# Kernel tuning notes

Hardware: AMD Instinct MI355X
Metric: run time of the kernel (lower is better)

Reference implementation:

```python
import jax, jax.numpy as jnp
import numpy as np

ALPHA_LIM = (float(np.exp(-1.0 / 5.0)), float(np.exp(-1.0 / 25.0)))
BETA_LIM = (float(np.exp(-1.0 / 30.0)), float(np.exp(-1.0 / 120.0)))
A_LIM = (-1.0, 1.0)
B_LIM = (0.0, 2.0)
THRESHOLD = 1.0


@jax.custom_vjp
def spike_boxcar(x):
    # Heaviside forward, boxcar surrogate gradient
    return (x > 0).astype(x.dtype)


def _spike_fwd(x):
    return spike_boxcar(x), x


def _spike_bwd(x, g):
    return (jnp.where(jnp.abs(x) <= 0.5, g, jnp.zeros_like(g)),)


spike_boxcar.defvjp(_spike_fwd, _spike_bwd)


def setup_inputs() -> dict:
    key = jax.random.key(0)
    ks = jax.random.split(key, 9)
    B, T, I, H = 128, 512, 512, 512
    return {
        "x": jax.random.normal(ks[0], (B, T, I), dtype=jnp.float32),
        "W": jax.random.normal(ks[1], (H, I), dtype=jnp.float32) / np.sqrt(I),
        "alpha": jax.random.uniform(ks[2], (H,), dtype=jnp.float32),
        "beta": jax.random.uniform(ks[3], (H,), dtype=jnp.float32),
        "a": jax.random.uniform(ks[4], (H,), dtype=jnp.float32),
        "b": jax.random.uniform(ks[5], (H,), dtype=jnp.float32),
        "u0": jax.random.uniform(ks[6], (B, H), dtype=jnp.float32),
        "w0": jax.random.uniform(ks[7], (B, H), dtype=jnp.float32),
        "s0": jax.random.uniform(ks[8], (B, H), dtype=jnp.float32),
    }


def reference(x, W, alpha, beta, a, b, u0, w0, s0):
    # x: [B, T, I]; W: [H, I] (nn.Linear weight, no bias)
    alpha = jnp.clip(alpha, ALPHA_LIM[0], ALPHA_LIM[1])
    beta = jnp.clip(beta, BETA_LIM[0], BETA_LIM[1])
    a = jnp.clip(a, A_LIM[0], A_LIM[1])
    b = jnp.clip(b, B_LIM[0], B_LIM[1])

    Wx = jnp.einsum("bti,hi->bth", x, W)  # [B, T, H]
    Wx_t = jnp.transpose(Wx, (1, 0, 2))    # [T, B, H] for scan over time

    def step(carry, wx_t):
        ut, wt, st = carry
        wt = beta * wt + a * ut + b * st
        ut = alpha * (ut - st) + (1.0 - alpha) * (wx_t - wt)
        st = spike_boxcar(ut - THRESHOLD)
        return (ut, wt, st), st

    _, s = jax.lax.scan(step, (u0, w0, s0), Wx_t)  # s: [T, B, H]
    return jnp.transpose(s, (1, 0, 2))  # [B, T, H]
```

## Files before the change

kernel.cpp:

```cpp
#include <hip/hip_runtime.h>
#include <hip/hip_bf16.h>


#define M_SZ 65536
#define H_SZ 512
#define K_SZ 512
#define B_SZ 128
#define T_SZ 512
#define LSTR 132

typedef __attribute__((ext_vector_type(4))) float f32x4;
typedef __attribute__((ext_vector_type(4))) unsigned int u32x4;

__device__ __forceinline__ bool detect_bf16(const unsigned int* __restrict__ w) {
  int c = 0;
#pragma unroll
  for (int i = 0; i < 64; ++i) {
    unsigned int e = (w[i] >> 7) & 0xffu;
    c += (e >= 115u && e <= 131u) ? 1 : 0;
  }
  return c > 32;
}

template <bool ISB>
__device__ __forceinline__ f32x4 ld4t(const void* __restrict__ p, size_t off) {
  if constexpr (!ISB) {
    return *reinterpret_cast<const f32x4*>(reinterpret_cast<const float*>(p) + off);
  } else {
    uint2 v = *reinterpret_cast<const uint2*>(reinterpret_cast<const unsigned short*>(p) + off);
    f32x4 r;
    r.x = __uint_as_float((v.x & 0xffffu) << 16);
    r.y = __uint_as_float(v.x & 0xffff0000u);
    r.z = __uint_as_float((v.y & 0xffffu) << 16);
    r.w = __uint_as_float(v.y & 0xffff0000u);
    return r;
  }
}

template <bool ISB>
__device__ __forceinline__ float ld1t(const void* __restrict__ p, int i) {
  if constexpr (!ISB) return reinterpret_cast<const float*>(p)[i];
  return __uint_as_float((unsigned int)(reinterpret_cast<const unsigned short*>(p)[i]) << 16);
}

__device__ __forceinline__ void gl_lds16(const void* g, void* l) {
  __builtin_amdgcn_global_load_lds(
      (const __attribute__((address_space(1))) void*)g,
      (__attribute__((address_space(3))) void*)l, 16, 0, 0);
}

template <bool ISB>
__device__ __forceinline__ void gemm_body(const void* __restrict__ X,
                                          const void* __restrict__ Wm,
                                          float* __restrict__ C,
                                          float* __restrict__ As,
                                          float* __restrict__ Bs) {
  const int tid = threadIdx.x;
  const int r0 = tid >> 2;
  const int q0 = (tid & 3) * 4;
  const int tx = tid & 15;
  const int ty = tid >> 4;
  const size_t M0 = (size_t)(blockIdx.x >> 2) * 128;
  const int N0 = (blockIdx.x & 3) * 128;

  float acc[8][8];
#pragma unroll
  for (int i = 0; i < 8; ++i)
#pragma unroll
    for (int j = 0; j < 8; ++j) acc[i][j] = 0.0f;

  const size_t aoff0 = (M0 + r0) * K_SZ + q0;
  const size_t aoff1 = (M0 + r0 + 64) * K_SZ + q0;
  const size_t boff0 = (size_t)(N0 + r0) * K_SZ + q0;
  const size_t boff1 = (size_t)(N0 + r0 + 64) * K_SZ + q0;

  f32x4 pa0 = ld4t<ISB>(X, aoff0), pa1 = ld4t<ISB>(X, aoff1);
  f32x4 pb0 = ld4t<ISB>(Wm, boff0), pb1 = ld4t<ISB>(Wm, boff1);

  for (int kk = 0; kk < K_SZ; kk += 16) {
    __syncthreads();
    As[(q0 + 0) * LSTR + r0] = pa0.x; As[(q0 + 1) * LSTR + r0] = pa0.y;
    As[(q0 + 2) * LSTR + r0] = pa0.z; As[(q0 + 3) * LSTR + r0] = pa0.w;
    As[(q0 + 0) * LSTR + r0 + 64] = pa1.x; As[(q0 + 1) * LSTR + r0 + 64] = pa1.y;
    As[(q0 + 2) * LSTR + r0 + 64] = pa1.z; As[(q0 + 3) * LSTR + r0 + 64] = pa1.w;
    Bs[(q0 + 0) * LSTR + r0] = pb0.x; Bs[(q0 + 1) * LSTR + r0] = pb0.y;
    Bs[(q0 + 2) * LSTR + r0] = pb0.z; Bs[(q0 + 3) * LSTR + r0] = pb0.w;
    Bs[(q0 + 0) * LSTR + r0 + 64] = pb1.x; Bs[(q0 + 1) * LSTR + r0 + 64] = pb1.y;
    Bs[(q0 + 2) * LSTR + r0 + 64] = pb1.z; Bs[(q0 + 3) * LSTR + r0 + 64] = pb1.w;
    __syncthreads();
    if (kk + 16 < K_SZ) {
      pa0 = ld4t<ISB>(X, aoff0 + kk + 16); pa1 = ld4t<ISB>(X, aoff1 + kk + 16);
      pb0 = ld4t<ISB>(Wm, boff0 + kk + 16); pb1 = ld4t<ISB>(Wm, boff1 + kk + 16);
    }
#pragma unroll
    for (int k = 0; k < 16; ++k) {
      const f32x4 a0 = *reinterpret_cast<const f32x4*>(As + k * LSTR + ty * 4);
      const f32x4 a1 = *reinterpret_cast<const f32x4*>(As + k * LSTR + 64 + ty * 4);
      const f32x4 b0 = *reinterpret_cast<const f32x4*>(Bs + k * LSTR + tx * 4);
      const f32x4 b1 = *reinterpret_cast<const f32x4*>(Bs + k * LSTR + 64 + tx * 4);
      const float av[8] = {a0.x, a0.y, a0.z, a0.w, a1.x, a1.y, a1.z, a1.w};
      const float bv[8] = {b0.x, b0.y, b0.z, b0.w, b1.x, b1.y, b1.z, b1.w};
#pragma unroll
      for (int i = 0; i < 8; ++i)
#pragma unroll
        for (int j = 0; j < 8; ++j) acc[i][j] += av[i] * bv[j];
    }
  }

#pragma unroll
  for (int r = 0; r < 8; ++r) {
    const size_t m = M0 + ((r < 4) ? (ty * 4 + r) : (64 + ty * 4 + (r - 4)));
    float* Cp = C + m * H_SZ + N0;
    f32x4 v0 = {acc[r][0], acc[r][1], acc[r][2], acc[r][3]};
    f32x4 v1 = {acc[r][4], acc[r][5], acc[r][6], acc[r][7]};
    __builtin_nontemporal_store(v0, reinterpret_cast<f32x4*>(Cp + tx * 4));
    __builtin_nontemporal_store(v1, reinterpret_cast<f32x4*>(Cp + 64 + tx * 4));
  }
}

__global__ __launch_bounds__(256) void sgemm_bt(const void* __restrict__ X,
                                                const void* __restrict__ Wm,
                                                float* __restrict__ C) {
  __shared__ float As[16 * LSTR];
  __shared__ float Bs[16 * LSTR];
  if (detect_bf16(reinterpret_cast<const unsigned int*>(X)))
    gemm_body<true>(X, Wm, C, As, Bs);
  else
    gemm_body<false>(X, Wm, C, As, Bs);
}

#define SG 8
#define NSG (T_SZ / SG)
#define RING 6

template <bool ISB>
__device__ __forceinline__ void scan_body(
    const float* __restrict__ wx, const void* __restrict__ alpha_p,
    const void* __restrict__ beta_p, const void* __restrict__ a_p,
    const void* __restrict__ b_p, const void* __restrict__ u0p,
    const void* __restrict__ w0p, const void* __restrict__ s0p,
    void* __restrict__ out, float* __restrict__ ring, float* __restrict__ stage) {
  const int tid = threadIdx.x;
  const int wave = tid >> 6;
  const int lane = tid & 63;
  const int gw = blockIdx.x * 4 + wave;
  const int b = gw >> 3;
  const int h0 = (gw & 7) * 64;
  const int h = h0 + lane;

  const float al = fminf(fmaxf(ld1t<ISB>(alpha_p, h), (float)0.8187307530779818),
                         (float)0.9607894391523232);
  const float be = fminf(fmaxf(ld1t<ISB>(beta_p, h), (float)0.9672161004820059),
                         (float)0.9917013044213351);
  const float av = fminf(fmaxf(ld1t<ISB>(a_p, h), -1.0f), 1.0f);
  const float bv = fminf(fmaxf(ld1t<ISB>(b_p, h), 0.0f), 2.0f);
  const float om = __fsub_rn(1.0f, al);

  const int bh = b * H_SZ + h;
  float u = ld1t<ISB>(u0p, bh);
  float w = ld1t<ISB>(w0p, bh);
  float s = ld1t<ISB>(s0p, bh);

  float* ring_w = ring + wave * (RING * SG * 64);
  float* stage_w = stage + wave * (2 * SG * 64);
  const float* wxb = wx + (size_t)b * T_SZ * H_SZ;

  auto issue_pair = [&](int g) {
    float* dst = ring_w + (g % RING) * (SG * 64);
#pragma unroll
    for (int j = 0; j < 2; ++j) {
      const int t = g * SG + j * 4 + (lane >> 4);
      gl_lds16(wxb + (size_t)t * H_SZ + h0 + (lane & 15) * 4, dst + j * 256);
    }
  };

#pragma unroll
  for (int g = 0; g < RING; ++g) issue_pair(g);

  __hip_bfloat16* outb = reinterpret_cast<__hip_bfloat16*>(out);
  float* outf = reinterpret_cast<float*>(out);

  for (int g = 0; g < NSG; ++g) {
    __builtin_amdgcn_s_waitcnt(0xF7A);
    __builtin_amdgcn_sched_barrier(0);

    const float* rb = ring_w + (g % RING) * (SG * 64);
    float* st = stage_w + (g & 1) * (SG * 64);
#pragma unroll
    for (int jt = 0; jt < SG; ++jt) {
      const float cur = rb[jt * 64 + lane];
      w = __fadd_rn(__fadd_rn(__fmul_rn(be, w), __fmul_rn(av, u)), __fmul_rn(bv, s));
      u = __fadd_rn(__fmul_rn(al, __fsub_rn(u, s)), __fmul_rn(om, __fsub_rn(cur, w)));
      s = (u > 1.0f) ? 1.0f : 0.0f;
      if constexpr (ISB)
        reinterpret_cast<unsigned short*>(st)[jt * 64 + lane] = (u > 1.0f) ? 0x3F80u : 0u;
      else
        st[jt * 64 + lane] = s;
    }
    if constexpr (ISB) {
      const u32x4 vv = *reinterpret_cast<const u32x4*>(
          reinterpret_cast<const char*>(st) + lane * 16);
      __hip_bfloat16* gp = outb + (size_t)b * T_SZ * H_SZ +
                           (size_t)(g * SG + (lane >> 3)) * H_SZ + h0 + (lane & 7) * 8;
      __builtin_nontemporal_store(vv, reinterpret_cast<u32x4*>(gp));
    } else {
#pragma unroll
      for (int k = 0; k < 2; ++k) {
        const u32x4 vv = *reinterpret_cast<const u32x4*>(
            reinterpret_cast<const char*>(st) + k * 1024 + lane * 16);
        float* gp = outf + (size_t)b * T_SZ * H_SZ +
                    (size_t)(g * SG + k * 4 + (lane >> 4)) * H_SZ + h0 + (lane & 15) * 4;
        __builtin_nontemporal_store(vv, reinterpret_cast<u32x4*>(gp));
      }
    }
    if (g + RING < NSG) issue_pair(g + RING);
  }
}

__global__ __launch_bounds__(256) void lif_scan(
    const float* __restrict__ wx, const void* __restrict__ X,
    const void* __restrict__ alpha_p, const void* __restrict__ beta_p,
    const void* __restrict__ a_p, const void* __restrict__ b_p,
    const void* __restrict__ u0p, const void* __restrict__ w0p,
    const void* __restrict__ s0p, void* __restrict__ out) {
  __shared__ float ring[4 * RING * SG * 64];
  __shared__ float stage[4 * 2 * SG * 64];
  if (detect_bf16(reinterpret_cast<const unsigned int*>(X)))
    scan_body<true>(wx, alpha_p, beta_p, a_p, b_p, u0p, w0p, s0p, out, ring, stage);
  else
    scan_body<false>(wx, alpha_p, beta_p, a_p, b_p, u0p, w0p, s0p, out, ring, stage);
}

extern "C" void kernel_launch(void* const* d_in, const int* in_sizes, int n_in,
                              void* d_out, int out_size, void* d_ws, size_t ws_size,
                              hipStream_t stream) {
  const void* X = d_in[0];
  const void* Wm = d_in[1];
  float* ws = reinterpret_cast<float*>(d_ws);

  sgemm_bt<<<dim3((M_SZ / 128) * (H_SZ / 128)), dim3(256), 0, stream>>>(X, Wm, ws);

  lif_scan<<<dim3(256), dim3(256), 0, stream>>>(
      ws, X, d_in[2], d_in[3], d_in[4], d_in[5], d_in[6], d_in[7], d_in[8], d_out);
}
```

Measured before the change: 649.9 us.

## Store GEMM output time-contiguous per neuron and scan from register prefetch

The GEMM epilogue now writes Wx transposed as [B, H, T], so each neuron's time series is contiguous in memory. The scan kernel gives each thread one (b,h) pair, reads 8 timesteps per vector load, and prefetches four chunks ahead in registers. This replaces the LDS ring buffer, async global-to-LDS loads and waitcnt pipeline. The trade-off is that GEMM stores become strided across rows with no nontemporal hint, and the scan now writes output as scalar per-timestep stores instead of staged 16-byte vectors.

```diff
diff --git a/kernel.cpp b/kernel.cpp
--- a/kernel.cpp
+++ b/kernel.cpp
@@ -10,7 +10,6 @@
 #define LSTR 132
 
 typedef __attribute__((ext_vector_type(4))) float f32x4;
-typedef __attribute__((ext_vector_type(4))) unsigned int u32x4;
 
 __device__ __forceinline__ bool detect_bf16(const unsigned int* __restrict__ w) {
   int c = 0;
@@ -41,12 +40,6 @@
 __device__ __forceinline__ float ld1t(const void* __restrict__ p, int i) {
   if constexpr (!ISB) return reinterpret_cast<const float*>(p)[i];
   return __uint_as_float((unsigned int)(reinterpret_cast<const unsigned short*>(p)[i]) << 16);
-}
-
-__device__ __forceinline__ void gl_lds16(const void* g, void* l) {
-  __builtin_amdgcn_global_load_lds(
-      (const __attribute__((address_space(1))) void*)g,
-      (__attribute__((address_space(3))) void*)l, 16, 0, 0);
 }
 
 template <bool ISB>
@@ -107,14 +100,16 @@
     }
   }
 
-#pragma unroll
-  for (int r = 0; r < 8; ++r) {
-    const size_t m = M0 + ((r < 4) ? (ty * 4 + r) : (64 + ty * 4 + (r - 4)));
-    float* Cp = C + m * H_SZ + N0;
-    f32x4 v0 = {acc[r][0], acc[r][1], acc[r][2], acc[r][3]};
-    f32x4 v1 = {acc[r][4], acc[r][5], acc[r][6], acc[r][7]};
-    __builtin_nontemporal_store(v0, reinterpret_cast<f32x4*>(Cp + tx * 4));
-    __builtin_nontemporal_store(v1, reinterpret_cast<f32x4*>(Cp + 64 + tx * 4));
+  const int b = (int)(M0 >> 9);
+  const int t0b = (int)(M0 & 511);
+#pragma unroll
+  for (int j = 0; j < 8; ++j) {
+    const int n = N0 + ((j < 4) ? (tx * 4 + j) : (64 + tx * 4 + (j - 4)));
+    float* cp = C + ((size_t)b * H_SZ + n) * T_SZ + t0b;
+    f32x4 vlo = {acc[0][j], acc[1][j], acc[2][j], acc[3][j]};
+    f32x4 vhi = {acc[4][j], acc[5][j], acc[6][j], acc[7][j]};
+    *reinterpret_cast<f32x4*>(cp + ty * 4) = vlo;
+    *reinterpret_cast<f32x4*>(cp + 64 + ty * 4) = vhi;
   }
 }
 
@@ -129,24 +124,17 @@
     gemm_body<false>(X, Wm, C, As, Bs);
 }
 
-#define SG 8
-#define NSG (T_SZ / SG)
-#define RING 6
-
 template <bool ISB>
 __device__ __forceinline__ void scan_body(
-    const float* __restrict__ wx, const void* __restrict__ alpha_p,
+    const float* __restrict__ wxT, const void* __restrict__ alpha_p,
     const void* __restrict__ beta_p, const void* __restrict__ a_p,
     const void* __restrict__ b_p, const void* __restrict__ u0p,
     const void* __restrict__ w0p, const void* __restrict__ s0p,
-    void* __restrict__ out, float* __restrict__ ring, float* __restrict__ stage) {
+    void* __restrict__ out) {
   const int tid = threadIdx.x;
-  const int wave = tid >> 6;
-  const int lane = tid & 63;
-  const int gw = blockIdx.x * 4 + wave;
-  const int b = gw >> 3;
-  const int h0 = (gw & 7) * 64;
-  const int h = h0 + lane;
+  const int bb = blockIdx.x >> 2;
+  const int quarter = blockIdx.x & 3;
+  const int h = quarter * 128 + tid;
 
   const float al = fminf(fmaxf(ld1t<ISB>(alpha_p, h), (float)0.8187307530779818),
                          (float)0.9607894391523232);
@@ -156,79 +144,57 @@
   const float bv = fminf(fmaxf(ld1t<ISB>(b_p, h), 0.0f), 2.0f);
   const float om = __fsub_rn(1.0f, al);
 
-  const int bh = b * H_SZ + h;
+  const int bh = bb * H_SZ + h;
   float u = ld1t<ISB>(u0p, bh);
   float w = ld1t<ISB>(w0p, bh);
   float s = ld1t<ISB>(s0p, bh);
 
-  float* ring_w = ring + wave * (RING * SG * 64);
-  float* stage_w = stage + wave * (2 * SG * 64);
-  const float* wxb = wx + (size_t)b * T_SZ * H_SZ;
-
-  auto issue_pair = [&](int g) {
-    float* dst = ring_w + (g % RING) * (SG * 64);
-#pragma unroll
-    for (int j = 0; j < 2; ++j) {
-      const int t = g * SG + j * 4 + (lane >> 4);
-      gl_lds16(wxb + (size_t)t * H_SZ + h0 + (lane & 15) * 4, dst + j * 256);
-    }
-  };
-
-#pragma unroll
-  for (int g = 0; g < RING; ++g) issue_pair(g);
-
+  const float* base = wxT + ((size_t)bb * H_SZ + h) * T_SZ;
+  float* outf = reinterpret_cast<float*>(out);
   __hip_bfloat16* outb = reinterpret_cast<__hip_bfloat16*>(out);
-  float* outf = reinterpret_cast<float*>(out);
-
-  for (int g = 0; g < NSG; ++g) {
-    __builtin_amdgcn_s_waitcnt(0xF7A);
-    __builtin_amdgcn_sched_barrier(0);
-
-    const float* rb = ring_w + (g % RING) * (SG * 64);
-    float* st = stage_w + (g & 1) * (SG * 64);
-#pragma unroll
-    for (int jt = 0; jt < SG; ++jt) {
-      const float cur = rb[jt * 64 + lane];
-      w = __fadd_rn(__fadd_rn(__fmul_rn(be, w), __fmul_rn(av, u)), __fmul_rn(bv, s));
-      u = __fadd_rn(__fmul_rn(al, __fsub_rn(u, s)), __fmul_rn(om, __fsub_rn(cur, w)));
-      s = (u > 1.0f) ? 1.0f : 0.0f;
-      if constexpr (ISB)
-        reinterpret_cast<unsigned short*>(st)[jt * 64 + lane] = (u > 1.0f) ? 0x3F80u : 0u;
-      else
-        st[jt * 64 + lane] = s;
-    }
-    if constexpr (ISB) {
-      const u32x4 vv = *reinterpret_cast<const u32x4*>(
-          reinterpret_cast<const char*>(st) + lane * 16);
-      __hip_bfloat16* gp = outb + (size_t)b * T_SZ * H_SZ +
-                           (size_t)(g * SG + (lane >> 3)) * H_SZ + h0 + (lane & 7) * 8;
-      __builtin_nontemporal_store(vv, reinterpret_cast<u32x4*>(gp));
-    } else {
-#pragma unroll
-      for (int k = 0; k < 2; ++k) {
-        const u32x4 vv = *reinterpret_cast<const u32x4*>(
-            reinterpret_cast<const char*>(st) + k * 1024 + lane * 16);
-        float* gp = outf + (size_t)b * T_SZ * H_SZ +
-                    (size_t)(g * SG + k * 4 + (lane >> 4)) * H_SZ + h0 + (lane & 15) * 4;
-        __builtin_nontemporal_store(vv, reinterpret_cast<u32x4*>(gp));
+  const size_t ob0 = (size_t)bb * T_SZ * H_SZ + h;
+
+  f32x4 ring[8];
+#pragma unroll
+  for (int c = 0; c < 4; ++c) {
+    ring[2 * c] = *reinterpret_cast<const f32x4*>(base + c * 8);
+    ring[2 * c + 1] = *reinterpret_cast<const f32x4*>(base + c * 8 + 4);
+  }
+
+  for (int c0 = 0; c0 < T_SZ / 8; c0 += 4) {
+#pragma unroll
+    for (int c2 = 0; c2 < 4; ++c2) {
+      const int c = c0 + c2;
+      const f32x4 v0 = ring[2 * c2];
+      const f32x4 v1 = ring[2 * c2 + 1];
+      if (c + 4 < T_SZ / 8) {
+        ring[2 * c2] = *reinterpret_cast<const f32x4*>(base + (c + 4) * 8);
+        ring[2 * c2 + 1] = *reinterpret_cast<const f32x4*>(base + (c + 4) * 8 + 4);
+      }
+      const float cur[8] = {v0.x, v0.y, v0.z, v0.w, v1.x, v1.y, v1.z, v1.w};
+#pragma unroll
+      for (int j = 0; j < 8; ++j) {
+        w = __fadd_rn(__fadd_rn(__fmul_rn(be, w), __fmul_rn(av, u)), __fmul_rn(bv, s));
+        u = __fadd_rn(__fmul_rn(al, __fsub_rn(u, s)), __fmul_rn(om, __fsub_rn(cur[j], w)));
+        s = (u > 1.0f) ? 1.0f : 0.0f;
+        const size_t o = ob0 + (size_t)(c * 8 + j) * H_SZ;
+        if constexpr (ISB) outb[o] = __float2bfloat16(s);
+        else outf[o] = s;
       }
     }
-    if (g + RING < NSG) issue_pair(g + RING);
-  }
-}
-
-__global__ __launch_bounds__(256) void lif_scan(
-    const float* __restrict__ wx, const void* __restrict__ X,
+  }
+}
+
+__global__ __launch_bounds__(128) void lif_scan(
+    const float* __restrict__ wxT, const void* __restrict__ X,
     const void* __restrict__ alpha_p, const void* __restrict__ beta_p,
     const void* __restrict__ a_p, const void* __restrict__ b_p,
     const void* __restrict__ u0p, const void* __restrict__ w0p,
     const void* __restrict__ s0p, void* __restrict__ out) {
-  __shared__ float ring[4 * RING * SG * 64];
-  __shared__ float stage[4 * 2 * SG * 64];
   if (detect_bf16(reinterpret_cast<const unsigned int*>(X)))
-    scan_body<true>(wx, alpha_p, beta_p, a_p, b_p, u0p, w0p, s0p, out, ring, stage);
+    scan_body<true>(wxT, alpha_p, beta_p, a_p, b_p, u0p, w0p, s0p, out);
   else
-    scan_body<false>(wx, alpha_p, beta_p, a_p, b_p, u0p, w0p, s0p, out, ring, stage);
+    scan_body<false>(wxT, alpha_p, beta_p, a_p, b_p, u0p, w0p, s0p, out);
 }
 
 extern "C" void kernel_launch(void* const* d_in, const int* in_sizes, int n_in,
@@ -240,6 +206,6 @@
 
   sgemm_bt<<<dim3((M_SZ / 128) * (H_SZ / 128)), dim3(256), 0, stream>>>(X, Wm, ws);
 
-  lif_scan<<<dim3(256), dim3(256), 0, stream>>>(
+  lif_scan<<<dim3(B_SZ * 4), dim3(128), 0, stream>>>(
       ws, X, d_in[2], d_in[3], d_in[4], d_in[5], d_in[6], d_in[7], d_in[8], d_out);
 }
```

After: 729.5 us. 1.12x slower.
